# Performance work log

Measured on AMD Instinct MI355X. Metric: run time of the kernel, lower is better.

The kernel has to match this reference:

```python
import jax, jax.numpy as jnp
import numpy as np

T = 2048          # num tokens
H_DIM = 2048      # hidden_size
NUM_HEADS = 32    # linear_num_value_heads
NUM_KV = 16       # linear_num_key_heads
DK = 128          # linear_key_head_dim
DV = 128          # linear_value_head_dim
KCONV = 4         # linear_conv_kernel_dim
KEY_DIM = NUM_KV * DK       # 2048
VAL_DIM = NUM_HEADS * DV    # 4096
CHUNK = 64


def setup_inputs() -> dict:
    key = jax.random.key(0)
    ks = jax.random.split(key, 14)
    s = 0.02
    return {
        "hidden_states": jax.random.normal(ks[0], (T, H_DIM), jnp.float32),
        "Wq": jax.random.normal(ks[1], (H_DIM, KEY_DIM), jnp.float32) * s,
        "Wk": jax.random.normal(ks[2], (H_DIM, KEY_DIM), jnp.float32) * s,
        "Wv": jax.random.normal(ks[3], (H_DIM, VAL_DIM), jnp.float32) * s,
        "Wa": jax.random.normal(ks[4], (H_DIM, NUM_HEADS), jnp.float32) * s,
        "Wb": jax.random.normal(ks[5], (H_DIM, NUM_HEADS), jnp.float32) * s,
        "Wg": jax.random.normal(ks[6], (H_DIM, VAL_DIM), jnp.float32) * s,
        "conv_q": jax.random.normal(ks[7], (KEY_DIM, KCONV), jnp.float32) * 0.3,
        "conv_k": jax.random.normal(ks[8], (KEY_DIM, KCONV), jnp.float32) * 0.3,
        "conv_v": jax.random.normal(ks[9], (VAL_DIM, KCONV), jnp.float32) * 0.3,
        "dt_bias": jax.random.normal(ks[10], (NUM_HEADS,), jnp.float32) * 0.1,
        "A_log": jnp.log(jax.random.uniform(ks[11], (NUM_HEADS,), jnp.float32, 1.0, 8.0)),
        "o_norm_weight": 1.0 + 0.1 * jax.random.normal(ks[12], (DV,), jnp.float32),
        "Wo": jax.random.normal(ks[13], (VAL_DIM, H_DIM), jnp.float32) * s,
    }


def _causal_depthwise_conv(x, w):
    # x: [T, C], w: [C, K] -> causal depthwise conv, output [T, C]
    K = w.shape[1]
    xp = jnp.pad(x, ((K - 1, 0), (0, 0)))
    out = jax.lax.conv_general_dilated(
        xp.T[None], w[:, None, :], window_strides=(1,), padding='VALID',
        dimension_numbers=('NCH', 'OIH', 'NCH'), feature_group_count=w.shape[0])
    return out[0].T


def _l2norm(x, eps=1e-6):
    return x * jax.lax.rsqrt(jnp.sum(x * x, axis=-1, keepdims=True) + eps)


def _gdn_core(q, k, v, g, beta):
    # q,k: [T,H,DK]; v: [T,H,DV]; g,beta: [T,H]. Gated delta-rule recurrence,
    # scanned in chunks (rematerialized inner scan = chunked selective scan).
    def step(S, inp):
        qt, kt, vt, gt, bt = inp
        S = S * jnp.exp(gt)[:, None, None]                  # decay state [H,DK,DV]
        kv = jnp.einsum('hk,hkv->hv', kt, S)                # read memory at k
        dv = bt[:, None] * (vt - kv)                        # delta update
        S = S + kt[:, :, None] * dv[:, None, :]             # write outer(k, dv)
        o = jnp.einsum('hk,hkv->hv', qt, S)                 # read at q
        return S, o

    def chunk_fn(S, ch):
        return jax.lax.scan(step, S, ch)

    def resh(x):
        return x.reshape(T // CHUNK, CHUNK, *x.shape[1:])

    xs = (resh(q), resh(k), resh(v), resh(g), resh(beta))
    S0 = jnp.zeros((NUM_HEADS, DK, DV), jnp.float32)
    _, o = jax.lax.scan(jax.checkpoint(chunk_fn), S0, xs)
    return o.reshape(T, NUM_HEADS, DV)


def reference(hidden_states, Wq, Wk, Wv, Wa, Wb, Wg, conv_q, conv_k, conv_v,
              dt_bias, A_log, o_norm_weight, Wo):
    h = hidden_states
    # projections
    mixed = jnp.concatenate([h @ Wq, h @ Wk, h @ Wv], axis=-1)
    # fused causal depthwise conv1d + silu over concatenated qkv
    wconv = jnp.concatenate([conv_q, conv_k, conv_v], axis=0)
    mixed = _causal_depthwise_conv(mixed, wconv)
    mixed = mixed * jax.nn.sigmoid(mixed)  # silu activation
    q, k, v = jnp.split(mixed, [KEY_DIM, 2 * KEY_DIM], axis=-1)
    q = q.reshape(T, NUM_KV, DK)
    k = k.reshape(T, NUM_KV, DK)
    v = v.reshape(T, NUM_HEADS, DV)
    ratio = NUM_HEADS // NUM_KV
    q = jnp.repeat(q, ratio, axis=1)   # GQA expand (repeat-interleave)
    k = jnp.repeat(k, ratio, axis=1)
    q = _l2norm(q)
    k = _l2norm(k)
    # fused gating: g = -exp(A_log) * softplus(a + dt_bias); beta = sigmoid(b)
    x = h @ Wa + dt_bias
    sp = jnp.where(x <= 20.0, jax.nn.softplus(x), x)  # threshold=20, beta=1
    g = -jnp.exp(A_log) * sp                          # [T, H]
    beta = jax.nn.sigmoid(h @ Wb)                     # allow_neg_eigval=False
    o = _gdn_core(q * (DK ** -0.5), k, v, g, beta)
    # gated RMSNorm (norm before gate), eps=1e-5
    gate = (h @ Wg).reshape(T, NUM_HEADS, DV)
    o = o * jax.lax.rsqrt(jnp.mean(o * o, axis=-1, keepdims=True) + 1e-5) * o_norm_weight
    o = o * (gate * jax.nn.sigmoid(gate))
    return o.reshape(T, VAL_DIM) @ Wo
```

## Files before the change

kernel.cpp:

```cpp
#include <hip/hip_runtime.h>
#include <hip/hip_bf16.h>
#include <stdint.h>
#include <stddef.h>

using bf16 = __hip_bfloat16;
typedef __attribute__((ext_vector_type(8))) short short8;
typedef __attribute__((ext_vector_type(4))) float f32x4;
typedef __attribute__((ext_vector_type(2))) float f32x2;

#define T_TOK 2048
#define HD    2048
#define NH    32
#define NKV   16
#define DKh   128
#define DVh   128

__device__ __forceinline__ void bf2f(uint32_t u, float& a, float& b) {
    union { uint32_t i; float f; } x;
    x.i = u << 16;          a = x.f;
    x.i = u & 0xffff0000u;  b = x.f;
}

__device__ __forceinline__ void gload16(const void* g, void* l) {
    __builtin_amdgcn_global_load_lds(
        (const __attribute__((address_space(1))) void*)g,
        (__attribute__((address_space(3))) void*)l, 16, 0, 0);
}

__device__ __forceinline__ void store_c(bf16* C, size_t off, float v) { C[off] = __float2bfloat16(v); }
__device__ __forceinline__ void store_c(float* C, size_t off, float v) { C[off] = v; }

template <int CTRL>
__device__ __forceinline__ float dppadd(float x) {
    int y = __builtin_amdgcn_update_dpp(0, __float_as_int(x), CTRL, 0xf, 0xf, true);
    return x + __int_as_float(y);
}
__device__ __forceinline__ void red16x2(float& x, float& y) {
    x = dppadd<0xB1>(x);  y = dppadd<0xB1>(y);
    x = dppadd<0x4E>(x);  y = dppadd<0x4E>(y);
    x = dppadd<0x141>(x); y = dppadd<0x141>(y);
    x = dppadd<0x140>(x); y = dppadd<0x140>(y);
}

__device__ __forceinline__ f32x2 pkfma(f32x2 a, f32x2 b, f32x2 c) {
    return __builtin_elementwise_fma(a, b, c);
}

__global__ __launch_bounds__(256) void f2b_kernel(
    const float* __restrict__ in, bf16* __restrict__ out, int n)
{
    int i = blockIdx.x * 256 + threadIdx.x;
    if (i < n) out[i] = __float2bfloat16(in[i]);
}

__global__ __launch_bounds__(256) void transpose_kernel(
    const float* __restrict__ in, bf16* __restrict__ out, int R, int C)
{
    __shared__ bf16 tile[32][33];
    int c0 = blockIdx.x * 32, r0 = blockIdx.y * 32;
    int x = threadIdx.x;
    int y = threadIdx.y;
    #pragma unroll
    for (int i = y; i < 32; i += 8)
        tile[i][x] = __float2bfloat16(in[(size_t)(r0 + i) * C + c0 + x]);
    __syncthreads();
    #pragma unroll
    for (int i = y; i < 32; i += 8)
        out[(size_t)(c0 + i) * R + r0 + x] = tile[x][i];
}

__global__ __launch_bounds__(256) void build_wab_kernel(
    const float* __restrict__ Wa, const float* __restrict__ Wb, bf16* __restrict__ out)
{
    int k = blockIdx.x * 256 + threadIdx.x;
    int n = blockIdx.y;
    float v = 0.f;
    if (n < 32)      v = Wa[(size_t)k * 32 + n];
    else if (n < 64) v = Wb[(size_t)k * 32 + (n - 32)];
    out[(size_t)n * 2048 + k] = __float2bfloat16(v);
}

template <typename OutT>
__global__ __launch_bounds__(256) void gemm_bt_kernel(
    const bf16* __restrict__ A, const bf16* __restrict__ B, OutT* __restrict__ C,
    int M, int N, int K)
{
    __shared__ short sA[128 * 64];
    __shared__ short sB[128 * 64];
    const int tid  = threadIdx.x;
    const int w    = tid >> 6;
    const int lane = tid & 63;
    const int quad = lane >> 4;
    const int r    = lane & 15;
    const int wm   = w >> 1, wn = w & 1;
    const int bm   = blockIdx.x, bn = blockIdx.y;
    const int lrow = lane >> 3;
    const int lp   = lane & 7;
    const int lc   = lp ^ lrow;

    f32x4 acc[4][4] = {};

    const int nkb = K >> 6;
    for (int kb = 0; kb < nkb; ++kb) {
        __syncthreads();
        #pragma unroll
        for (int it = 0; it < 4; ++it) {
            int grp = w * 4 + it;
            int rr  = grp * 8 + lrow;
            const bf16* ga = A + (size_t)(bm * 128 + rr) * K + kb * 64 + lc * 8;
            gload16(ga, (void*)(sA + grp * 512));
            const bf16* gb = B + (size_t)(bn * 128 + rr) * K + kb * 64 + lc * 8;
            gload16(gb, (void*)(sB + grp * 512));
        }
        __syncthreads();

        #pragma unroll
        for (int kk = 0; kk < 2; ++kk) {
            short8 av[4], bv[4];
            #pragma unroll
            for (int i = 0; i < 4; ++i) {
                int p   = (kk * 4 + quad) ^ (r & 7);
                int row = wm * 64 + i * 16 + r;
                av[i] = *(const short8*)(sA + row * 64 + p * 8);
                int rowb = wn * 64 + i * 16 + r;
                bv[i] = *(const short8*)(sB + rowb * 64 + p * 8);
            }
            #pragma unroll
            for (int i = 0; i < 4; ++i)
                #pragma unroll
                for (int j = 0; j < 4; ++j)
                    acc[i][j] = __builtin_amdgcn_mfma_f32_16x16x32_bf16(
                        av[i], bv[j], acc[i][j], 0, 0, 0);
        }
    }

    #pragma unroll
    for (int i = 0; i < 4; ++i) {
        int row0 = bm * 128 + wm * 64 + i * 16 + quad * 4;
        #pragma unroll
        for (int j = 0; j < 4; ++j) {
            int col = bn * 128 + wn * 64 + j * 16 + r;
            #pragma unroll
            for (int e = 0; e < 4; ++e)
                store_c(C, (size_t)(row0 + e) * N + col, acc[i][j][e]);
        }
    }
}

__global__ __launch_bounds__(128) void conv_qk_kernel(
    const bf16* __restrict__ mixed, const float* __restrict__ cq,
    const float* __restrict__ ck, float* __restrict__ qn, float* __restrict__ kn,
    float* __restrict__ pk4)
{
    int t   = blockIdx.x;
    int hkv = blockIdx.y;
    int d   = threadIdx.x;
    int cl  = hkv * DKh + d;
    float aq = 0.f, ak = 0.f;
    #pragma unroll
    for (int j = 0; j < 4; ++j) {
        int ts = t - 3 + j;
        if (ts >= 0) {
            aq += __bfloat162float(mixed[(size_t)ts * 8192 + cl])        * cq[cl * 4 + j];
            ak += __bfloat162float(mixed[(size_t)ts * 8192 + 2048 + cl]) * ck[cl * 4 + j];
        }
    }
    float sq = aq / (1.f + __expf(-aq));
    float sk = ak / (1.f + __expf(-ak));
    float s0 = sq * sq, s1 = sk * sk, s2 = sq * sk;
    #pragma unroll
    for (int m = 1; m < 64; m <<= 1) {
        s0 += __shfl_xor(s0, m, 64);
        s1 += __shfl_xor(s1, m, 64);
        s2 += __shfl_xor(s2, m, 64);
    }
    __shared__ float part[6];
    if ((threadIdx.x & 63) == 0) {
        int w = threadIdx.x >> 6;
        part[w * 3 + 0] = s0; part[w * 3 + 1] = s1; part[w * 3 + 2] = s2;
    }
    __syncthreads();
    float sumq = part[0] + part[3];
    float sumk = part[1] + part[4];
    float sqk  = part[2] + part[5];
    float rnq = rsqrtf(sumq + 1e-6f);
    float rnk = rsqrtf(sumk + 1e-6f);
    const float scale = 0.08838834764831845f;
    qn[(size_t)t * 2048 + cl] = sq * rnq * scale;
    kn[(size_t)t * 2048 + cl] = sk * rnk;
    if (d == 0) {
        float qk = sqk * rnq * rnk * scale;
        pk4[((size_t)t * 32 + 2 * hkv)     * 4 + 3] = qk;
        pk4[((size_t)t * 32 + 2 * hkv + 1) * 4 + 3] = qk;
    }
}

__global__ __launch_bounds__(256) void conv_v_kernel(
    const bf16* __restrict__ mixed, const float* __restrict__ cv, bf16* __restrict__ vv)
{
    int idx = blockIdx.x * 256 + threadIdx.x;
    int t = idx >> 12, c = idx & 4095;
    float acc = 0.f;
    #pragma unroll
    for (int j = 0; j < 4; ++j) {
        int ts = t - 3 + j;
        if (ts >= 0)
            acc += __bfloat162float(mixed[(size_t)ts * 8192 + 4096 + c]) * cv[c * 4 + j];
    }
    vv[idx] = __float2bfloat16(acc / (1.f + __expf(-acc)));
}

__global__ __launch_bounds__(256) void gating_kernel(
    const float* __restrict__ ab, const float* __restrict__ dt_bias,
    const float* __restrict__ A_log, float* __restrict__ pk4)
{
    int i = blockIdx.x * 256 + threadIdx.x;
    int t = i >> 5, h = i & 31;
    float a  = ab[(size_t)t * 128 + h] + dt_bias[h];
    float sp = (a <= 20.f) ? log1pf(__expf(a)) : a;
    float gg = -__expf(A_log[h]) * sp;
    float b  = ab[(size_t)t * 128 + 32 + h];
    float eg = __expf(gg);
    float be = 1.f / (1.f + __expf(-b));
    pk4[(size_t)i * 4 + 0] = eg;
    pk4[(size_t)i * 4 + 1] = -be * eg;
    pk4[(size_t)i * 4 + 2] = be;
}

__device__ __forceinline__ void gdn_step(
    f32x2 S[4], float4 kfa, float4 kfb, float4 qfa, float4 qfb,
    float egt, float nbt, float bvt, float qkt, bf16* optr, bool writer)
{
    f32x2 k2[4] = {{kfa.x, kfa.y}, {kfa.z, kfa.w}, {kfb.x, kfb.y}, {kfb.z, kfb.w}};
    f32x2 q2[4] = {{qfa.x, qfa.y}, {qfa.z, qfa.w}, {qfb.x, qfb.y}, {qfb.z, qfb.w}};
    f32x2 pd = pkfma(S[1], k2[1], S[0] * k2[0]);
    f32x2 pe = pkfma(S[3], k2[3], S[2] * k2[2]);
    f32x2 qd = pkfma(S[1], q2[1], S[0] * q2[0]);
    f32x2 qe = pkfma(S[3], q2[3], S[2] * q2[2]);
    f32x2 e2 = {egt, egt};
    f32x2 Se0 = S[0] * e2, Se1 = S[1] * e2, Se2 = S[2] * e2, Se3 = S[3] * e2;
    f32x2 ps = pd + pe;
    f32x2 qs = qd + qe;
    float d1 = ps.x + ps.y;
    float d2 = qs.x + qs.y;
    red16x2(d1, d2);
    float dvv = fmaf(nbt, d1, bvt);
    f32x2 dv2 = {dvv, dvv};
    S[0] = pkfma(k2[0], dv2, Se0);
    S[1] = pkfma(k2[1], dv2, Se1);
    S[2] = pkfma(k2[2], dv2, Se2);
    S[3] = pkfma(k2[3], dv2, Se3);
    if (writer) *optr = __float2bfloat16(fmaf(qkt, dvv, egt * d2));
}

#define PF_DEPTH 8

__global__ __launch_bounds__(256, 1) void recur_kernel(
    const float* __restrict__ qn, const float* __restrict__ kn, const bf16* __restrict__ vv,
    const float* __restrict__ pk4, bf16* __restrict__ o)
{
    int h   = blockIdx.x;
    int sp  = blockIdx.y;
    int tid = threadIdx.x;
    int dvl = tid >> 4;
    int dkg = tid & 15;
    int dv  = sp * 16 + dvl;
    int hkv = h >> 1;
    bool writer = (dkg == 0);

    const float* kp = kn + hkv * DKh + dkg * 8;
    const float* qp = qn + hkv * DKh + dkg * 8;
    const bf16*  vp = vv + h * DVh + dv;
    const float* gp = pk4 + h * 4;
    bf16* optr = o + h * DVh + dv;

    f32x2 S[4] = {{0.f, 0.f}, {0.f, 0.f}, {0.f, 0.f}, {0.f, 0.f}};

    float4 ka[PF_DEPTH], kb[PF_DEPTH], qa[PF_DEPTH], qb[PF_DEPTH];
    float  es[PF_DEPTH], ns[PF_DEPTH], qs[PF_DEPTH], bv[PF_DEPTH];
    #pragma unroll
    for (int s = 0; s < PF_DEPTH; ++s) {
        ka[s] = *(const float4*)(kp + (size_t)s * 2048);
        kb[s] = *(const float4*)(kp + (size_t)s * 2048 + 4);
        qa[s] = *(const float4*)(qp + (size_t)s * 2048);
        qb[s] = *(const float4*)(qp + (size_t)s * 2048 + 4);
        float4 g4 = *(const float4*)(gp + (size_t)s * 128);
        float vcf = __bfloat162float(vp[(size_t)s * 4096]);
        es[s] = g4.x; ns[s] = g4.y; qs[s] = g4.w; bv[s] = g4.z * vcf;
    }
    const float* kl = kp + (size_t)PF_DEPTH * 2048;
    const float* ql = qp + (size_t)PF_DEPTH * 2048;
    const bf16*  vl = vp + (size_t)PF_DEPTH * 4096;
    const float* gl = gp + (size_t)PF_DEPTH * 128;

    #pragma unroll 1
    for (int t = 0; t < T_TOK; t += PF_DEPTH) {
        #pragma unroll
        for (int s = 0; s < PF_DEPTH; ++s) {
            float4 kfa = ka[s], kfb = kb[s], qfa = qa[s], qfb = qb[s];
            float egt = es[s], nbt = ns[s], qkt = qs[s], bvt = bv[s];
            ka[s] = *(const float4*)(kl + (size_t)s * 2048);
            kb[s] = *(const float4*)(kl + (size_t)s * 2048 + 4);
            qa[s] = *(const float4*)(ql + (size_t)s * 2048);
            qb[s] = *(const float4*)(ql + (size_t)s * 2048 + 4);
            float4 g4 = *(const float4*)(gl + (size_t)s * 128);
            float vcf = __bfloat162float(vl[(size_t)s * 4096]);
            es[s] = g4.x; ns[s] = g4.y; qs[s] = g4.w; bv[s] = g4.z * vcf;
            gdn_step(S, kfa, kfb, qfa, qfb, egt, nbt, bvt, qkt,
                     optr + (size_t)(t + s) * 4096, writer);
        }
        kl += (size_t)PF_DEPTH * 2048;
        ql += (size_t)PF_DEPTH * 2048;
        vl += (size_t)PF_DEPTH * 4096;
        gl += (size_t)PF_DEPTH * 128;
    }
}

__global__ __launch_bounds__(256) void normgate_kernel(
    const bf16* __restrict__ o, const bf16* __restrict__ gate,
    const float* __restrict__ w, bf16* __restrict__ og)
{
    int grp  = blockIdx.x * 4 + (threadIdx.x >> 6);
    int lane = threadIdx.x & 63;
    int t = grp >> 5, h = grp & 31;
    size_t base = (size_t)t * 4096 + h * DVh;
    uint32_t uo = *(const uint32_t*)(o + base + lane * 2);
    float a, b; bf2f(uo, a, b);
    float ss = a * a + b * b;
    #pragma unroll
    for (int m = 1; m < 64; m <<= 1) ss += __shfl_xor(ss, m, 64);
    float rn = rsqrtf(ss * (1.f / 128.f) + 1e-5f);
    uint32_t ug = *(const uint32_t*)(gate + base + lane * 2);
    float ga, gb; bf2f(ug, ga, gb);
    float wa = w[lane * 2], wb = w[lane * 2 + 1];
    float oa = a * rn * wa * (ga / (1.f + __expf(-ga)));
    float ob = b * rn * wb * (gb / (1.f + __expf(-gb)));
    og[base + lane * 2]     = __float2bfloat16(oa);
    og[base + lane * 2 + 1] = __float2bfloat16(ob);
}

extern "C" void kernel_launch(void* const* d_in, const int* in_sizes, int n_in,
                              void* d_out, int out_size, void* d_ws, size_t ws_size,
                              hipStream_t stream)
{
    const float* h       = (const float*)d_in[0];
    const float* Wq      = (const float*)d_in[1];
    const float* Wk      = (const float*)d_in[2];
    const float* Wv      = (const float*)d_in[3];
    const float* Wa      = (const float*)d_in[4];
    const float* Wb      = (const float*)d_in[5];
    const float* Wg      = (const float*)d_in[6];
    const float* conv_q  = (const float*)d_in[7];
    const float* conv_k  = (const float*)d_in[8];
    const float* conv_v  = (const float*)d_in[9];
    const float* dt_bias = (const float*)d_in[10];
    const float* A_log   = (const float*)d_in[11];
    const float* onw     = (const float*)d_in[12];
    const float* Wo      = (const float*)d_in[13];
    float* out = (float*)d_out;

    char* ws = (char*)d_ws;
    bf16*  WqkvT = (bf16*)ws;   ws += (size_t)8192 * 2048 * 2;
    bf16*  WgT   = (bf16*)ws;   ws += (size_t)4096 * 2048 * 2;
    bf16*  WoT   = (bf16*)ws;   ws += (size_t)2048 * 4096 * 2;
    bf16*  WabT  = (bf16*)ws;   ws += (size_t)128 * 2048 * 2;
    bf16*  hb    = (bf16*)ws;   ws += (size_t)2048 * 2048 * 2;
    bf16*  mixed = (bf16*)ws;   ws += (size_t)2048 * 8192 * 2;
    float* ab    = (float*)ws;  ws += (size_t)2048 * 128 * 4;
    float* knb   = (float*)ws;  ws += (size_t)2048 * 2048 * 4;
    bf16*  vvb   = (bf16*)ws;   ws += (size_t)2048 * 4096 * 2;
    float* pk4   = (float*)ws;  ws += (size_t)2048 * 32 * 4 * 4;
    ws += 32768;
    float* qnb = (float*)WgT;
    bf16*  ob   = WqkvT;
    bf16*  gate = WqkvT + (size_t)2048 * 4096;
    bf16*  og   = mixed;

    dim3 tb(32, 8);
    transpose_kernel<<<dim3(64, 64),  tb, 0, stream>>>(Wq, WqkvT,                       2048, 2048);
    transpose_kernel<<<dim3(64, 64),  tb, 0, stream>>>(Wk, WqkvT + (size_t)2048 * 2048, 2048, 2048);
    transpose_kernel<<<dim3(128, 64), tb, 0, stream>>>(Wv, WqkvT + (size_t)4096 * 2048, 2048, 4096);
    transpose_kernel<<<dim3(128, 64), tb, 0, stream>>>(Wg, WgT,                         2048, 4096);
    transpose_kernel<<<dim3(64, 128), tb, 0, stream>>>(Wo, WoT,                         4096, 2048);
    build_wab_kernel<<<dim3(8, 128), 256, 0, stream>>>(Wa, Wb, WabT);
    f2b_kernel<<<16384, 256, 0, stream>>>(h, hb, 2048 * 2048);

    gemm_bt_kernel<bf16> <<<dim3(16, 64), 256, 0, stream>>>(hb, WqkvT, mixed, 2048, 8192, 2048);
    gemm_bt_kernel<float><<<dim3(16, 1),  256, 0, stream>>>(hb, WabT,  ab,    2048, 128,  2048);
    gemm_bt_kernel<bf16> <<<dim3(16, 32), 256, 0, stream>>>(hb, WgT,   gate,  2048, 4096, 2048);

    conv_qk_kernel<<<dim3(2048, 16), 128, 0, stream>>>(mixed, conv_q, conv_k, qnb, knb, pk4);
    conv_v_kernel<<<32768, 256, 0, stream>>>(mixed, conv_v, vvb);
    gating_kernel<<<256, 256, 0, stream>>>(ab, dt_bias, A_log, pk4);

    recur_kernel<<<dim3(32, 8), 256, 0, stream>>>(qnb, knb, vvb, pk4, ob);
    normgate_kernel<<<16384, 256, 0, stream>>>(ob, gate, onw, og);

    gemm_bt_kernel<float><<<dim3(16, 16), 256, 0, stream>>>(og, WoT, out, 2048, 2048, 4096);
}
```

Baseline: 960.4 us.

## Process two value columns per thread in recurrence and stage gates in LDS

The recurrence kernel now has each thread own two value columns, so blocks drop from 256 to 128 threads and every loaded k/q vector is reused across two state columns. Four DPP reductions are interleaved per step to shorten the dependency chain. The per-head gate parameters are transposed to a head-major layout and preloaded into shared memory, which takes gate loads off the global path. The prefetch depth is reduced to 4 to hold the larger register state, at the cost of fewer total waves hiding latency.

New measurement: 1.122 ms. 16.9% more time.

```diff
diff --git a/kernel.cpp b/kernel.cpp
--- a/kernel.cpp
+++ b/kernel.cpp
@@ -35,16 +35,17 @@
     int y = __builtin_amdgcn_update_dpp(0, __float_as_int(x), CTRL, 0xf, 0xf, true);
     return x + __int_as_float(y);
 }
-__device__ __forceinline__ void red16x2(float& x, float& y) {
-    x = dppadd<0xB1>(x);  y = dppadd<0xB1>(y);
-    x = dppadd<0x4E>(x);  y = dppadd<0x4E>(y);
-    x = dppadd<0x141>(x); y = dppadd<0x141>(y);
-    x = dppadd<0x140>(x); y = dppadd<0x140>(y);
+__device__ __forceinline__ void red16x4(float& a, float& b, float& c, float& d) {
+    a = dppadd<0xB1>(a);  b = dppadd<0xB1>(b);  c = dppadd<0xB1>(c);  d = dppadd<0xB1>(d);
+    a = dppadd<0x4E>(a);  b = dppadd<0x4E>(b);  c = dppadd<0x4E>(c);  d = dppadd<0x4E>(d);
+    a = dppadd<0x141>(a); b = dppadd<0x141>(b); c = dppadd<0x141>(c); d = dppadd<0x141>(d);
+    a = dppadd<0x140>(a); b = dppadd<0x140>(b); c = dppadd<0x140>(c); d = dppadd<0x140>(d);
 }
 
 __device__ __forceinline__ f32x2 pkfma(f32x2 a, f32x2 b, f32x2 c) {
     return __builtin_elementwise_fma(a, b, c);
 }
+__device__ __forceinline__ f32x2 sp2(float x) { return f32x2{x, x}; }
 
 __global__ __launch_bounds__(256) void f2b_kernel(
     const float* __restrict__ in, bf16* __restrict__ out, int n)
@@ -190,8 +191,8 @@
     kn[(size_t)t * 2048 + cl] = sk * rnk;
     if (d == 0) {
         float qk = sqk * rnq * rnk * scale;
-        pk4[((size_t)t * 32 + 2 * hkv)     * 4 + 3] = qk;
-        pk4[((size_t)t * 32 + 2 * hkv + 1) * 4 + 3] = qk;
+        pk4[((size_t)(2 * hkv)     * T_TOK + t) * 4 + 3] = qk;
+        pk4[((size_t)(2 * hkv + 1) * T_TOK + t) * 4 + 3] = qk;
     }
 }
 
@@ -215,104 +216,131 @@
     const float* __restrict__ A_log, float* __restrict__ pk4)
 {
     int i = blockIdx.x * 256 + threadIdx.x;
-    int t = i >> 5, h = i & 31;
+    int h = i >> 11, t = i & 2047;
     float a  = ab[(size_t)t * 128 + h] + dt_bias[h];
     float sp = (a <= 20.f) ? log1pf(__expf(a)) : a;
     float gg = -__expf(A_log[h]) * sp;
     float b  = ab[(size_t)t * 128 + 32 + h];
     float eg = __expf(gg);
     float be = 1.f / (1.f + __expf(-b));
-    pk4[(size_t)i * 4 + 0] = eg;
-    pk4[(size_t)i * 4 + 1] = -be * eg;
-    pk4[(size_t)i * 4 + 2] = be;
+    size_t base = ((size_t)h * T_TOK + t) * 4;
+    pk4[base + 0] = eg;
+    pk4[base + 1] = -be * eg;
+    pk4[base + 2] = be;
 }
 
 __device__ __forceinline__ void gdn_step(
-    f32x2 S[4], float4 kfa, float4 kfb, float4 qfa, float4 qfb,
-    float egt, float nbt, float bvt, float qkt, bf16* optr, bool writer)
-{
-    f32x2 k2[4] = {{kfa.x, kfa.y}, {kfa.z, kfa.w}, {kfb.x, kfb.y}, {kfb.z, kfb.w}};
-    f32x2 q2[4] = {{qfa.x, qfa.y}, {qfa.z, qfa.w}, {qfb.x, qfb.y}, {qfb.z, qfb.w}};
-    f32x2 pd = pkfma(S[1], k2[1], S[0] * k2[0]);
-    f32x2 pe = pkfma(S[3], k2[3], S[2] * k2[2]);
-    f32x2 qd = pkfma(S[1], q2[1], S[0] * q2[0]);
-    f32x2 qe = pkfma(S[3], q2[3], S[2] * q2[2]);
-    f32x2 e2 = {egt, egt};
-    f32x2 Se0 = S[0] * e2, Se1 = S[1] * e2, Se2 = S[2] * e2, Se3 = S[3] * e2;
-    f32x2 ps = pd + pe;
-    f32x2 qs = qd + qe;
-    float d1 = ps.x + ps.y;
-    float d2 = qs.x + qs.y;
-    red16x2(d1, d2);
-    float dvv = fmaf(nbt, d1, bvt);
-    f32x2 dv2 = {dvv, dvv};
-    S[0] = pkfma(k2[0], dv2, Se0);
-    S[1] = pkfma(k2[1], dv2, Se1);
-    S[2] = pkfma(k2[2], dv2, Se2);
-    S[3] = pkfma(k2[3], dv2, Se3);
-    if (writer) *optr = __float2bfloat16(fmaf(qkt, dvv, egt * d2));
-}
-
-#define PF_DEPTH 8
-
-__global__ __launch_bounds__(256, 1) void recur_kernel(
+    f32x2 S[8], const float kf[8], const float qf[8],
+    float es, float ns, float qk, float bv0, float bv1,
+    uint32_t* optr, bool writer)
+{
+    f32x2 pa = S[0] * sp2(kf[0]);
+    f32x2 pb = S[1] * sp2(kf[1]);
+    f32x2 qa_ = S[0] * sp2(qf[0]);
+    f32x2 qb_ = S[1] * sp2(qf[1]);
+    pa = pkfma(S[2], sp2(kf[2]), pa);  pb = pkfma(S[3], sp2(kf[3]), pb);
+    qa_ = pkfma(S[2], sp2(qf[2]), qa_); qb_ = pkfma(S[3], sp2(qf[3]), qb_);
+    pa = pkfma(S[4], sp2(kf[4]), pa);  pb = pkfma(S[5], sp2(kf[5]), pb);
+    qa_ = pkfma(S[4], sp2(qf[4]), qa_); qb_ = pkfma(S[5], sp2(qf[5]), qb_);
+    pa = pkfma(S[6], sp2(kf[6]), pa);  pb = pkfma(S[7], sp2(kf[7]), pb);
+    qa_ = pkfma(S[6], sp2(qf[6]), qa_); qb_ = pkfma(S[7], sp2(qf[7]), qb_);
+    f32x2 d1 = pa + pb;
+    f32x2 d2 = qa_ + qb_;
+    float d1a = d1.x, d1b = d1.y, d2a = d2.x, d2b = d2.y;
+    f32x2 e2 = sp2(es);
+    f32x2 Se[8];
+    #pragma unroll
+    for (int j = 0; j < 8; ++j) Se[j] = S[j] * e2;
+    red16x4(d1a, d1b, d2a, d2b);
+    float dvv0 = fmaf(ns, d1a, bv0);
+    float dvv1 = fmaf(ns, d1b, bv1);
+    f32x2 dv2 = {dvv0, dvv1};
+    #pragma unroll
+    for (int j = 0; j < 8; ++j) S[j] = pkfma(sp2(kf[j]), dv2, Se[j]);
+    if (writer) {
+        float o0 = fmaf(qk, dvv0, es * d2a);
+        float o1 = fmaf(qk, dvv1, es * d2b);
+        union { bf16 h2[2]; uint32_t u; } p;
+        p.h2[0] = __float2bfloat16(o0);
+        p.h2[1] = __float2bfloat16(o1);
+        *optr = p.u;
+    }
+}
+
+#define PF_DEPTH 4
+
+__global__ __launch_bounds__(128, 1) void recur_kernel(
     const float* __restrict__ qn, const float* __restrict__ kn, const bf16* __restrict__ vv,
     const float* __restrict__ pk4, bf16* __restrict__ o)
 {
+    __shared__ float sgate[(T_TOK + PF_DEPTH) * 4];
     int h   = blockIdx.x;
     int sp  = blockIdx.y;
     int tid = threadIdx.x;
     int dvl = tid >> 4;
     int dkg = tid & 15;
-    int dv  = sp * 16 + dvl;
+    int dv0 = sp * 16 + dvl * 2;
     int hkv = h >> 1;
     bool writer = (dkg == 0);
 
-    const float* kp = kn + hkv * DKh + dkg * 8;
-    const float* qp = qn + hkv * DKh + dkg * 8;
-    const bf16*  vp = vv + h * DVh + dv;
-    const float* gp = pk4 + h * 4;
-    bf16* optr = o + h * DVh + dv;
-
-    f32x2 S[4] = {{0.f, 0.f}, {0.f, 0.f}, {0.f, 0.f}, {0.f, 0.f}};
+    {
+        const float* gp = pk4 + (size_t)h * T_TOK * 4;
+        for (int i = tid; i < T_TOK; i += 128)
+            *(float4*)(sgate + (size_t)i * 4) = *(const float4*)(gp + (size_t)i * 4);
+        if (tid < PF_DEPTH * 4) sgate[T_TOK * 4 + tid] = 0.f;
+    }
+    __syncthreads();
+
+    const float*    kp   = kn + hkv * DKh + dkg * 8;
+    const float*    qp   = qn + hkv * DKh + dkg * 8;
+    const uint32_t* vp   = (const uint32_t*)(vv + h * DVh + dv0);
+    uint32_t*       ob32 = (uint32_t*)(o + h * DVh + dv0);
+
+    f32x2 S[8] = {};
 
     float4 ka[PF_DEPTH], kb[PF_DEPTH], qa[PF_DEPTH], qb[PF_DEPTH];
-    float  es[PF_DEPTH], ns[PF_DEPTH], qs[PF_DEPTH], bv[PF_DEPTH];
+    float  es_[PF_DEPTH], ns_[PF_DEPTH], qs_[PF_DEPTH], b0_[PF_DEPTH], b1_[PF_DEPTH];
     #pragma unroll
     for (int s = 0; s < PF_DEPTH; ++s) {
         ka[s] = *(const float4*)(kp + (size_t)s * 2048);
         kb[s] = *(const float4*)(kp + (size_t)s * 2048 + 4);
         qa[s] = *(const float4*)(qp + (size_t)s * 2048);
         qb[s] = *(const float4*)(qp + (size_t)s * 2048 + 4);
-        float4 g4 = *(const float4*)(gp + (size_t)s * 128);
-        float vcf = __bfloat162float(vp[(size_t)s * 4096]);
-        es[s] = g4.x; ns[s] = g4.y; qs[s] = g4.w; bv[s] = g4.z * vcf;
-    }
-    const float* kl = kp + (size_t)PF_DEPTH * 2048;
-    const float* ql = qp + (size_t)PF_DEPTH * 2048;
-    const bf16*  vl = vp + (size_t)PF_DEPTH * 4096;
-    const float* gl = gp + (size_t)PF_DEPTH * 128;
+        float4 g4 = *(const float4*)(sgate + (size_t)s * 4);
+        uint32_t vu = vp[(size_t)s * 2048];
+        float v0f, v1f; bf2f(vu, v0f, v1f);
+        es_[s] = g4.x; ns_[s] = g4.y; qs_[s] = g4.w;
+        b0_[s] = g4.z * v0f; b1_[s] = g4.z * v1f;
+    }
+    const float*    kl = kp + (size_t)PF_DEPTH * 2048;
+    const float*    ql = qp + (size_t)PF_DEPTH * 2048;
+    const uint32_t* vl = vp + (size_t)PF_DEPTH * 2048;
 
     #pragma unroll 1
     for (int t = 0; t < T_TOK; t += PF_DEPTH) {
         #pragma unroll
         for (int s = 0; s < PF_DEPTH; ++s) {
-            float4 kfa = ka[s], kfb = kb[s], qfa = qa[s], qfb = qb[s];
-            float egt = es[s], nbt = ns[s], qkt = qs[s], bvt = bv[s];
+            float kf[8] = {ka[s].x, ka[s].y, ka[s].z, ka[s].w,
+                           kb[s].x, kb[s].y, kb[s].z, kb[s].w};
+            float qf[8] = {qa[s].x, qa[s].y, qa[s].z, qa[s].w,
+                           qb[s].x, qb[s].y, qb[s].z, qb[s].w};
+            float egt = es_[s], nbt = ns_[s], qkt = qs_[s];
+            float bv0 = b0_[s], bv1 = b1_[s];
             ka[s] = *(const float4*)(kl + (size_t)s * 2048);
             kb[s] = *(const float4*)(kl + (size_t)s * 2048 + 4);
             qa[s] = *(const float4*)(ql + (size_t)s * 2048);
             qb[s] = *(const float4*)(ql + (size_t)s * 2048 + 4);
-            float4 g4 = *(const float4*)(gl + (size_t)s * 128);
-            float vcf = __bfloat162float(vl[(size_t)s * 4096]);
-            es[s] = g4.x; ns[s] = g4.y; qs[s] = g4.w; bv[s] = g4.z * vcf;
-            gdn_step(S, kfa, kfb, qfa, qfb, egt, nbt, bvt, qkt,
-                     optr + (size_t)(t + s) * 4096, writer);
+            float4 g4 = *(const float4*)(sgate + (size_t)(t + s + PF_DEPTH) * 4);
+            uint32_t vu = vl[(size_t)s * 2048];
+            float v0f, v1f; bf2f(vu, v0f, v1f);
+            es_[s] = g4.x; ns_[s] = g4.y; qs_[s] = g4.w;
+            b0_[s] = g4.z * v0f; b1_[s] = g4.z * v1f;
+            gdn_step(S, kf, qf, egt, nbt, qkt, bv0, bv1,
+                     ob32 + (size_t)(t + s) * 2048, writer);
         }
         kl += (size_t)PF_DEPTH * 2048;
         ql += (size_t)PF_DEPTH * 2048;
-        vl += (size_t)PF_DEPTH * 4096;
-        gl += (size_t)PF_DEPTH * 128;
+        vl += (size_t)PF_DEPTH * 2048;
     }
 }
 
@@ -369,7 +397,7 @@
     float* ab    = (float*)ws;  ws += (size_t)2048 * 128 * 4;
     float* knb   = (float*)ws;  ws += (size_t)2048 * 2048 * 4;
     bf16*  vvb   = (bf16*)ws;   ws += (size_t)2048 * 4096 * 2;
-    float* pk4   = (float*)ws;  ws += (size_t)2048 * 32 * 4 * 4;
+    float* pk4   = (float*)ws;  ws += (size_t)NH * T_TOK * 4 * 4;
     ws += 32768;
     float* qnb = (float*)WgT;
     bf16*  ob   = WqkvT;
@@ -393,7 +421,7 @@
     conv_v_kernel<<<32768, 256, 0, stream>>>(mixed, conv_v, vvb);
     gating_kernel<<<256, 256, 0, stream>>>(ab, dt_bias, A_log, pk4);
 
-    recur_kernel<<<dim3(32, 8), 256, 0, stream>>>(qnb, knb, vvb, pk4, ob);
+    recur_kernel<<<dim3(32, 8), 128, 0, stream>>>(qnb, knb, vvb, pk4, ob);
     normgate_kernel<<<16384, 256, 0, stream>>>(ob, gate, onw, og);
 
     gemm_bt_kernel<float><<<dim3(16, 16), 256, 0, stream>>>(og, WoT, out, 2048, 2048, 4096);
```

## Stage recurrence k/q/v/gates through double-buffered LDS tiles with head-major gates

Applied to the files above, without the earlier changes.

The recurrence kernel stops prefetching k, q, gate and v values per thread into registers from global memory. Instead, each block cooperatively copies 16-token tiles into double-buffered shared memory using global_load_lds, with one barrier per tile. The per-step gate array is transposed to head-major layout so each head's gates are contiguous for that copy. This removes redundant global loads across threads that share the same k/q, and frees registers. In exchange it adds a block-wide barrier per tile, and the final prefetch reads past the end of the buffers into adjacent workspace.

Result: no change. 951.6 us (-0.9%).

```diff
diff --git a/kernel.cpp b/kernel.cpp
--- a/kernel.cpp
+++ b/kernel.cpp
@@ -190,8 +190,8 @@
     kn[(size_t)t * 2048 + cl] = sk * rnk;
     if (d == 0) {
         float qk = sqk * rnq * rnk * scale;
-        pk4[((size_t)t * 32 + 2 * hkv)     * 4 + 3] = qk;
-        pk4[((size_t)t * 32 + 2 * hkv + 1) * 4 + 3] = qk;
+        pk4[((size_t)(2 * hkv)     * T_TOK + t) * 4 + 3] = qk;
+        pk4[((size_t)(2 * hkv + 1) * T_TOK + t) * 4 + 3] = qk;
     }
 }
 
@@ -215,16 +215,17 @@
     const float* __restrict__ A_log, float* __restrict__ pk4)
 {
     int i = blockIdx.x * 256 + threadIdx.x;
-    int t = i >> 5, h = i & 31;
+    int h = i >> 11, t = i & 2047;
     float a  = ab[(size_t)t * 128 + h] + dt_bias[h];
     float sp = (a <= 20.f) ? log1pf(__expf(a)) : a;
     float gg = -__expf(A_log[h]) * sp;
     float b  = ab[(size_t)t * 128 + 32 + h];
     float eg = __expf(gg);
     float be = 1.f / (1.f + __expf(-b));
-    pk4[(size_t)i * 4 + 0] = eg;
-    pk4[(size_t)i * 4 + 1] = -be * eg;
-    pk4[(size_t)i * 4 + 2] = be;
+    size_t base = ((size_t)h * T_TOK + t) * 4;
+    pk4[base + 0] = eg;
+    pk4[base + 1] = -be * eg;
+    pk4[base + 2] = be;
 }
 
 __device__ __forceinline__ void gdn_step(
@@ -253,66 +254,75 @@
     if (writer) *optr = __float2bfloat16(fmaf(qkt, dvv, egt * d2));
 }
 
-#define PF_DEPTH 8
+#define TILE 16
 
 __global__ __launch_bounds__(256, 1) void recur_kernel(
     const float* __restrict__ qn, const float* __restrict__ kn, const bf16* __restrict__ vv,
     const float* __restrict__ pk4, bf16* __restrict__ o)
 {
-    int h   = blockIdx.x;
-    int sp  = blockIdx.y;
-    int tid = threadIdx.x;
-    int dvl = tid >> 4;
-    int dkg = tid & 15;
-    int dv  = sp * 16 + dvl;
-    int hkv = h >> 1;
+    __shared__ float    skq[2][TILE][256];
+    __shared__ float    sgt[2][TILE][4];
+    __shared__ uint16_t sv2[2][TILE][16];
+
+    int h    = blockIdx.x;
+    int sp   = blockIdx.y;
+    int tid  = threadIdx.x;
+    int dvl  = tid >> 4;
+    int dkg  = tid & 15;
+    int dv   = sp * 16 + dvl;
+    int hkv  = h >> 1;
+    int wave = tid >> 6;
+    int lane = tid & 63;
     bool writer = (dkg == 0);
 
-    const float* kp = kn + hkv * DKh + dkg * 8;
-    const float* qp = qn + hkv * DKh + dkg * 8;
-    const bf16*  vp = vv + h * DVh + dv;
-    const float* gp = pk4 + h * 4;
-    bf16* optr = o + h * DVh + dv;
-
-    f32x2 S[4] = {{0.f, 0.f}, {0.f, 0.f}, {0.f, 0.f}, {0.f, 0.f}};
-
-    float4 ka[PF_DEPTH], kb[PF_DEPTH], qa[PF_DEPTH], qb[PF_DEPTH];
-    float  es[PF_DEPTH], ns[PF_DEPTH], qs[PF_DEPTH], bv[PF_DEPTH];
-    #pragma unroll
-    for (int s = 0; s < PF_DEPTH; ++s) {
-        ka[s] = *(const float4*)(kp + (size_t)s * 2048);
-        kb[s] = *(const float4*)(kp + (size_t)s * 2048 + 4);
-        qa[s] = *(const float4*)(qp + (size_t)s * 2048);
-        qb[s] = *(const float4*)(qp + (size_t)s * 2048 + 4);
-        float4 g4 = *(const float4*)(gp + (size_t)s * 128);
-        float vcf = __bfloat162float(vp[(size_t)s * 4096]);
-        es[s] = g4.x; ns[s] = g4.y; qs[s] = g4.w; bv[s] = g4.z * vcf;
-    }
-    const float* kl = kp + (size_t)PF_DEPTH * 2048;
-    const float* ql = qp + (size_t)PF_DEPTH * 2048;
-    const bf16*  vl = vp + (size_t)PF_DEPTH * 4096;
-    const float* gl = gp + (size_t)PF_DEPTH * 128;
-
+    bf16* optr = o + (size_t)h * DVh + dv;
+
+    const float* kqsrc = (lane < 32)
+        ? (kn + (size_t)hkv * DKh + (size_t)lane * 4)
+        : (qn + (size_t)hkv * DKh + (size_t)(lane - 32) * 4);
+    const bf16*  vsrc  = vv + (size_t)h * DVh + sp * 16 + (size_t)(lane & 1) * 8;
+    const float* gsrc  = pk4 + ((size_t)h * T_TOK) * 4;
+
+    f32x2 S[4] = {};
+
+    auto stage = [&](int b, int t0) {
+        #pragma unroll
+        for (int i = 0; i < 4; ++i) {
+            int tok = wave * 4 + i;
+            gload16(kqsrc + (size_t)(t0 + tok) * 2048, (void*)&skq[b][tok][0]);
+        }
+        if (wave == 0) {
+            if (lane < 32)
+                gload16(vsrc + (size_t)(t0 + (lane >> 1)) * 4096, (void*)&sv2[b][0][0]);
+        } else if (wave == 1) {
+            if (lane < 16)
+                gload16(gsrc + (size_t)(t0 + lane) * 4, (void*)&sgt[b][0][0]);
+        }
+    };
+
+    stage(0, 0);
+    __syncthreads();
+
+    int buf = 0;
     #pragma unroll 1
-    for (int t = 0; t < T_TOK; t += PF_DEPTH) {
+    for (int t0 = 0; t0 < T_TOK; t0 += TILE) {
+        stage(buf ^ 1, t0 + TILE);
         #pragma unroll
-        for (int s = 0; s < PF_DEPTH; ++s) {
-            float4 kfa = ka[s], kfb = kb[s], qfa = qa[s], qfb = qb[s];
-            float egt = es[s], nbt = ns[s], qkt = qs[s], bvt = bv[s];
-            ka[s] = *(const float4*)(kl + (size_t)s * 2048);
-            kb[s] = *(const float4*)(kl + (size_t)s * 2048 + 4);
-            qa[s] = *(const float4*)(ql + (size_t)s * 2048);
-            qb[s] = *(const float4*)(ql + (size_t)s * 2048 + 4);
-            float4 g4 = *(const float4*)(gl + (size_t)s * 128);
-            float vcf = __bfloat162float(vl[(size_t)s * 4096]);
-            es[s] = g4.x; ns[s] = g4.y; qs[s] = g4.w; bv[s] = g4.z * vcf;
-            gdn_step(S, kfa, kfb, qfa, qfb, egt, nbt, bvt, qkt,
-                     optr + (size_t)(t + s) * 4096, writer);
-        }
-        kl += (size_t)PF_DEPTH * 2048;
-        ql += (size_t)PF_DEPTH * 2048;
-        vl += (size_t)PF_DEPTH * 4096;
-        gl += (size_t)PF_DEPTH * 128;
+        for (int s = 0; s < TILE; ++s) {
+            const float* tokp = &skq[buf][s][0];
+            float4 kA = *(const float4*)(tokp + dkg * 4);
+            float4 kB = *(const float4*)(tokp + 64 + dkg * 4);
+            float4 qA = *(const float4*)(tokp + 128 + dkg * 4);
+            float4 qB = *(const float4*)(tokp + 192 + dkg * 4);
+            float4 g4 = *(const float4*)(&sgt[buf][s][0]);
+            uint32_t vu = sv2[buf][s][dvl];
+            float vf = __uint_as_float(vu << 16);
+            float bvt = g4.z * vf;
+            gdn_step(S, kA, kB, qA, qB, g4.x, g4.y, bvt, g4.w,
+                     optr + (size_t)(t0 + s) * 4096, writer);
+        }
+        __syncthreads();
+        buf ^= 1;
     }
 }
 
@@ -369,7 +379,7 @@
     float* ab    = (float*)ws;  ws += (size_t)2048 * 128 * 4;
     float* knb   = (float*)ws;  ws += (size_t)2048 * 2048 * 4;
     bf16*  vvb   = (bf16*)ws;   ws += (size_t)2048 * 4096 * 2;
-    float* pk4   = (float*)ws;  ws += (size_t)2048 * 32 * 4 * 4;
+    float* pk4   = (float*)ws;  ws += (size_t)NH * T_TOK * 4 * 4;
     ws += 32768;
     float* qnb = (float*)WgT;
     bf16*  ob   = WqkvT;
```
